# Optimization experiments

Hardware: AMD Instinct MI355X
Metric: run time of the kernel (lower is better)

Reference implementation:

```python
import jax, jax.numpy as jnp
import numpy as np

B, N, H, HEADS = 4, 512, 256, 8
SUBH = H // HEADS
FF = 4 * H
EPS = 1e-5


def _layernorm(x, g, b):
    m = jnp.mean(x, axis=-1, keepdims=True)
    v = jnp.mean(jnp.square(x - m), axis=-1, keepdims=True)
    return (x - m) * jax.lax.rsqrt(v + EPS) * g + b


def setup_inputs() -> dict:
    key = jax.random.key(0)
    ks = jax.random.split(key, 10)
    sc = 0.02
    return {
        "S": jax.random.normal(ks[0], (B, N, H), dtype=jnp.float32),
        "T": jax.random.normal(ks[1], (B, N, N, H), dtype=jnp.float32),
        "masks": jnp.ones((B, N), dtype=bool),
        "Wqk": jax.random.normal(ks[2], (H, HEADS), dtype=jnp.float32) * sc,
        "Wv": jax.random.normal(ks[3], (H, H), dtype=jnp.float32) * sc,
        "bv": jnp.zeros((H,), dtype=jnp.float32),
        "Wo": jax.random.normal(ks[4], (H, H), dtype=jnp.float32) * sc,
        "bo": jnp.zeros((H,), dtype=jnp.float32),
        "g0": jnp.ones((H,), dtype=jnp.float32),
        "beta0": jnp.zeros((H,), dtype=jnp.float32),
        "W1": jax.random.normal(ks[5], (H, FF), dtype=jnp.float32) * sc,
        "b1": jnp.zeros((FF,), dtype=jnp.float32),
        "W2": jax.random.normal(ks[6], (FF, H), dtype=jnp.float32) * sc,
        "b2": jnp.zeros((H,), dtype=jnp.float32),
        "g1": jnp.ones((H,), dtype=jnp.float32),
        "beta1": jnp.zeros((H,), dtype=jnp.float32),
    }


def reference(S, T, masks, Wqk, Wv, bv, Wo, bo, g0, beta0, W1, b1, W2, b2, g1, beta1):
    # pairwise mask: [B,N,N], additive -1000 where masked
    mask2 = masks[:, None, :] & masks[:, :, None]
    add = -1000.0 * (1.0 - mask2.astype(jnp.float32))

    # attention scores: linear projection of pairwise tensor T -> [B, heads, N, N]
    attn = jnp.einsum('bije,eh->bhij', T, Wqk) + add[:, None, :, :]
    attn = jax.nn.softmax(attn, axis=-1)

    # values: [B, heads, N, subH]
    v = (S @ Wv + bv).reshape(B, N, HEADS, SUBH).transpose(0, 2, 1, 3)
    ctx = jnp.einsum('bhij,bhjd->bhid', attn, v)  # [B, heads, N, subH]
    ctx = ctx.transpose(0, 2, 1, 3).reshape(B, N, H)

    x = jax.nn.relu(ctx @ Wo + bo)
    x = _layernorm(S + x, g0, beta0)

    y = jax.nn.relu(x @ W1 + b1) @ W2 + b2
    out = _layernorm(x + y, g1, beta1)
    return (out, attn)
```

## Files before the change

### kernel.cpp

```cpp
#include <hip/hip_runtime.h>
#include <hip/hip_bf16.h>
#include <cstddef>

#define NB 4
#define NN 512
#define NH 256
#define NHEADS 8
#define NSUBH 32
#define NFF 1024
#define LNEPS 1e-5f

using short8 = __attribute__((ext_vector_type(8))) short;
using f32x4  = __attribute__((ext_vector_type(4))) float;
using fvec4  = __attribute__((ext_vector_type(4))) float;

__device__ __forceinline__ unsigned short f2bf(float x) {
    __hip_bfloat16 h = __float2bfloat16(x);
    return *reinterpret_cast<unsigned short*>(&h);
}

__global__ __launch_bounds__(64) void prep_wqk_kernel(
    const float* __restrict__ Wqk, short8* __restrict__ wqk_bf)
{
    const int lane = threadIdx.x;
    const int n = lane & 15;
    #pragma unroll
    for (int ks = 0; ks < 8; ++ks) {
        short8 v;
        #pragma unroll
        for (int q = 0; q < 8; ++q) {
            const int k = ks * 32 + ((lane >> 4) & 3) * 8 + q;
            v[q] = (n < 8) ? (short)f2bf(Wqk[k * NHEADS + n]) : (short)0;
        }
        wqk_bf[ks * 64 + lane] = v;
    }
}

__global__ __launch_bounds__(256) void vproj_kernel(
    const float* __restrict__ S, const float* __restrict__ Wv,
    const float* __restrict__ bv, float* __restrict__ v_ws)
{
    __shared__ float srow[8][NH];
    const int t = threadIdx.x;
    const int row0 = blockIdx.x * 8;
    #pragma unroll
    for (int r = 0; r < 8; ++r) srow[r][t] = S[(size_t)(row0 + r) * NH + t];
    __syncthreads();

    float acc[8];
    #pragma unroll
    for (int r = 0; r < 8; ++r) acc[r] = 0.0f;
    for (int e = 0; e < NH; e += 4) {
        const float w0 = Wv[(size_t)(e + 0) * NH + t];
        const float w1 = Wv[(size_t)(e + 1) * NH + t];
        const float w2 = Wv[(size_t)(e + 2) * NH + t];
        const float w3 = Wv[(size_t)(e + 3) * NH + t];
        #pragma unroll
        for (int r = 0; r < 8; ++r) {
            const float4 x4 = *(const float4*)&srow[r][e];
            acc[r] = fmaf(x4.x, w0, fmaf(x4.y, w1, fmaf(x4.z, w2, fmaf(x4.w, w3, acc[r]))));
        }
    }
    const float bvc = bv[t];
    const int h = t >> 5, d = t & 31;
    const int b = row0 / NN;
    const int jbase = row0 & (NN - 1);
    #pragma unroll
    for (int r = 0; r < 8; ++r)
        v_ws[((size_t)(b * NHEADS + h) * NN + (size_t)(jbase + r)) * NSUBH + d] = acc[r] + bvc;
}

__global__ __launch_bounds__(256, 4) void scores_kernel(
    const float* __restrict__ T, const short8* __restrict__ wqk_bf,
    float* __restrict__ scores)
{
    __shared__ unsigned short tlds[64 * 256];
    const int t = threadIdx.x;
    const int lane = t & 63, wv = t >> 6;
    const int bi = blockIdx.x >> 3;
    const int jt = blockIdx.x & 7;
    const int jbase = jt * 64;

    const fvec4* Tv = (const fvec4*)(T + ((size_t)bi * NN + jbase) * NH);

    fvec4 ga[16];
    #pragma unroll
    for (int i = 0; i < 16; ++i)
        ga[i] = __builtin_nontemporal_load(&Tv[(size_t)(16 * wv + i) * 64 + lane]);

    short8 bfrag[8];
    #pragma unroll
    for (int ks = 0; ks < 8; ++ks) bfrag[ks] = wqk_bf[ks * 64 + lane];

    #pragma unroll
    for (int i = 0; i < 16; ++i) {
        const int row = 16 * wv + i;
        unsigned short v[4];
        v[0] = f2bf(ga[i][0]); v[1] = f2bf(ga[i][1]);
        v[2] = f2bf(ga[i][2]); v[3] = f2bf(ga[i][3]);
        const int byte = (row * 512 + lane * 8) ^ ((row & 7) << 4);
        *(uint2*)((char*)tlds + byte) = *(const uint2*)v;
    }

    f32x4 acc = {0.0f, 0.0f, 0.0f, 0.0f};
    const int jr = 16 * wv + (lane & 15);
    #pragma unroll
    for (int ks = 0; ks < 8; ++ks) {
        const int byte = (jr * 512 + ks * 64 + (lane >> 4) * 16) ^ ((jr & 7) << 4);
        const short8 af = *(const short8*)((const char*)tlds + byte);
        acc = __builtin_amdgcn_mfma_f32_16x16x32_bf16(af, bfrag[ks], acc, 0, 0, 0);
    }

    const int h = lane & 15;
    if (h < 8) {
        const int b = bi >> 9, i = bi & (NN - 1);
        const int j0 = jbase + 16 * wv + (lane >> 4) * 4;
        float4 st;
        st.x = acc[0]; st.y = acc[1]; st.z = acc[2]; st.w = acc[3];
        *(float4*)&scores[((size_t)(b * NHEADS + h) * NN + i) * NN + j0] = st;
    }
}

__global__ __launch_bounds__(256) void softmax_ctx_kernel(
    const int* __restrict__ masks, const float* __restrict__ v_ws,
    float* __restrict__ attn, float* __restrict__ ctx_out)
{
    __shared__ float sc[NN][9];
    __shared__ float maddv[NN];
    const int t = threadIdx.x;
    const int b = blockIdx.x >> 9;
    const int i = blockIdx.x & (NN - 1);

    const int mi = masks[b * NN + i];
    for (int j = t; j < NN; j += 256)
        maddv[j] = (mi != 0 && masks[b * NN + j] != 0) ? 0.0f : -1000.0f;
    __syncthreads();

    const int h = t >> 5;
    const int l32 = t & 31;
    float* srow = attn + ((size_t)(b * NHEADS + h) * NN + i) * NN;

    float vals[16];
    float m = -1e30f;
    #pragma unroll
    for (int k = 0; k < 4; ++k) {
        const int j0 = 4 * l32 + 128 * k;
        float4 s4 = *(const float4*)&srow[j0];
        const float4 m4 = *(const float4*)&maddv[j0];
        s4.x += m4.x; s4.y += m4.y; s4.z += m4.z; s4.w += m4.w;
        vals[4 * k + 0] = s4.x; vals[4 * k + 1] = s4.y;
        vals[4 * k + 2] = s4.z; vals[4 * k + 3] = s4.w;
        m = fmaxf(m, fmaxf(fmaxf(s4.x, s4.y), fmaxf(s4.z, s4.w)));
    }
    #pragma unroll
    for (int off = 16; off >= 1; off >>= 1) m = fmaxf(m, __shfl_xor(m, off, 32));
    float sum = 0.0f;
    #pragma unroll
    for (int k = 0; k < 16; ++k) {
        const float e = __expf(vals[k] - m);
        vals[k] = e;
        sum += e;
    }
    #pragma unroll
    for (int off = 16; off >= 1; off >>= 1) sum += __shfl_xor(sum, off, 32);
    const float inv = 1.0f / sum;
    #pragma unroll
    for (int k = 0; k < 4; ++k) {
        const int j0 = 4 * l32 + 128 * k;
        float4 p4;
        p4.x = vals[4 * k + 0] * inv; p4.y = vals[4 * k + 1] * inv;
        p4.z = vals[4 * k + 2] * inv; p4.w = vals[4 * k + 3] * inv;
        *(float4*)&srow[j0] = p4;
        sc[j0 + 0][h] = p4.x; sc[j0 + 1][h] = p4.y;
        sc[j0 + 2][h] = p4.z; sc[j0 + 3][h] = p4.w;
    }
    __syncthreads();

    const int d = l32;
    const float* vp = v_ws + (size_t)(b * NHEADS + h) * NN * NSUBH + d;
    float acc = 0.0f;
    #pragma unroll 8
    for (int j = 0; j < NN; ++j)
        acc = fmaf(sc[j][h], vp[(size_t)j * NSUBH], acc);
    ctx_out[(size_t)(b * NN + i) * NH + h * NSUBH + d] = acc;
}

__global__ __launch_bounds__(256) void tail_kernel(
    const float* __restrict__ ctx, const float* __restrict__ S,
    const float* __restrict__ Wo, const float* __restrict__ bo,
    const float* __restrict__ g0, const float* __restrict__ beta0,
    const float* __restrict__ W1, const float* __restrict__ b1,
    const float* __restrict__ W2, const float* __restrict__ b2,
    const float* __restrict__ g1, const float* __restrict__ beta1,
    float* __restrict__ out)
{
    __shared__ float xin[8][NH];
    __shared__ float x1[8][NH];
    __shared__ float ybuf[8][NFF];
    const int t = threadIdx.x;
    const int row0 = blockIdx.x * 8;

    #pragma unroll
    for (int r = 0; r < 8; ++r) xin[r][t] = ctx[(size_t)(row0 + r) * NH + t];
    __syncthreads();

    float acc[8];
    #pragma unroll
    for (int r = 0; r < 8; ++r) acc[r] = 0.0f;
    for (int e = 0; e < NH; e += 4) {
        const float w0 = Wo[(size_t)(e + 0) * NH + t];
        const float w1 = Wo[(size_t)(e + 1) * NH + t];
        const float w2 = Wo[(size_t)(e + 2) * NH + t];
        const float w3 = Wo[(size_t)(e + 3) * NH + t];
        #pragma unroll
        for (int r = 0; r < 8; ++r) {
            const float4 x4 = *(const float4*)&xin[r][e];
            acc[r] = fmaf(x4.x, w0, fmaf(x4.y, w1, fmaf(x4.z, w2, fmaf(x4.w, w3, acc[r]))));
        }
    }
    const float boc = bo[t];
    #pragma unroll
    for (int r = 0; r < 8; ++r) {
        const float xv = fmaxf(acc[r] + boc, 0.0f);
        x1[r][t] = S[(size_t)(row0 + r) * NH + t] + xv;
    }
    __syncthreads();

    {
        const int wv = t >> 6, ln = t & 63;
        #pragma unroll
        for (int rr = 0; rr < 2; ++rr) {
            const int r = wv * 2 + rr;
            float s1 = 0.0f, s2 = 0.0f;
            #pragma unroll
            for (int k = 0; k < 4; ++k) {
                const float z = x1[r][ln + 64 * k];
                s1 += z; s2 += z * z;
            }
            #pragma unroll
            for (int off = 32; off >= 1; off >>= 1) {
                s1 += __shfl_xor(s1, off);
                s2 += __shfl_xor(s2, off);
            }
            const float mu = s1 * (1.0f / NH);
            const float rsig = rsqrtf(s2 * (1.0f / NH) - mu * mu + LNEPS);
            #pragma unroll
            for (int k = 0; k < 4; ++k) {
                const int c = ln + 64 * k;
                x1[r][c] = (x1[r][c] - mu) * rsig * g0[c] + beta0[c];
            }
        }
    }
    __syncthreads();

    float acc2[8][4];
    #pragma unroll
    for (int r = 0; r < 8; ++r)
        #pragma unroll
        for (int q = 0; q < 4; ++q) acc2[r][q] = 0.0f;
    for (int e = 0; e < NH; e += 4) {
        float4 x4[8];
        #pragma unroll
        for (int r = 0; r < 8; ++r) x4[r] = *(const float4*)&x1[r][e];
        #pragma unroll
        for (int q = 0; q < 4; ++q) {
            const float* wc = W1 + (size_t)e * NFF + (t + 256 * q);
            const float w0 = wc[0 * NFF], w1 = wc[1 * NFF], w2 = wc[2 * NFF], w3 = wc[3 * NFF];
            #pragma unroll
            for (int r = 0; r < 8; ++r)
                acc2[r][q] = fmaf(x4[r].x, w0, fmaf(x4[r].y, w1, fmaf(x4[r].z, w2, fmaf(x4[r].w, w3, acc2[r][q]))));
        }
    }
    #pragma unroll
    for (int q = 0; q < 4; ++q) {
        const float b1c = b1[t + 256 * q];
        #pragma unroll
        for (int r = 0; r < 8; ++r)
            ybuf[r][t + 256 * q] = fmaxf(acc2[r][q] + b1c, 0.0f);
    }
    __syncthreads();

    float acc3[8];
    #pragma unroll
    for (int r = 0; r < 8; ++r) acc3[r] = 0.0f;
    for (int f = 0; f < NFF; f += 4) {
        const float w0 = W2[(size_t)(f + 0) * NH + t];
        const float w1 = W2[(size_t)(f + 1) * NH + t];
        const float w2 = W2[(size_t)(f + 2) * NH + t];
        const float w3 = W2[(size_t)(f + 3) * NH + t];
        #pragma unroll
        for (int r = 0; r < 8; ++r) {
            const float4 y4 = *(const float4*)&ybuf[r][f];
            acc3[r] = fmaf(y4.x, w0, fmaf(y4.y, w1, fmaf(y4.z, w2, fmaf(y4.w, w3, acc3[r]))));
        }
    }
    const float b2c = b2[t];
    #pragma unroll
    for (int r = 0; r < 8; ++r)
        xin[r][t] = x1[r][t] + acc3[r] + b2c;
    __syncthreads();

    {
        const int wv = t >> 6, ln = t & 63;
        #pragma unroll
        for (int rr = 0; rr < 2; ++rr) {
            const int r = wv * 2 + rr;
            float s1 = 0.0f, s2 = 0.0f;
            #pragma unroll
            for (int k = 0; k < 4; ++k) {
                const float z = xin[r][ln + 64 * k];
                s1 += z; s2 += z * z;
            }
            #pragma unroll
            for (int off = 32; off >= 1; off >>= 1) {
                s1 += __shfl_xor(s1, off);
                s2 += __shfl_xor(s2, off);
            }
            const float mu = s1 * (1.0f / NH);
            const float rsig = rsqrtf(s2 * (1.0f / NH) - mu * mu + LNEPS);
            #pragma unroll
            for (int k = 0; k < 4; ++k) {
                const int c = ln + 64 * k;
                out[(size_t)(row0 + r) * NH + c] = (xin[r][c] - mu) * rsig * g1[c] + beta1[c];
            }
        }
    }
}

extern "C" void kernel_launch(void* const* d_in, const int* in_sizes, int n_in,
                              void* d_out, int out_size, void* d_ws, size_t ws_size,
                              hipStream_t stream) {
    const float* S     = (const float*)d_in[0];
    const float* T     = (const float*)d_in[1];
    const int*   masks = (const int*)  d_in[2];
    const float* Wqk   = (const float*)d_in[3];
    const float* Wv    = (const float*)d_in[4];
    const float* bv    = (const float*)d_in[5];
    const float* Wo    = (const float*)d_in[6];
    const float* bo    = (const float*)d_in[7];
    const float* g0    = (const float*)d_in[8];
    const float* beta0 = (const float*)d_in[9];
    const float* W1    = (const float*)d_in[10];
    const float* b1    = (const float*)d_in[11];
    const float* W2    = (const float*)d_in[12];
    const float* b2    = (const float*)d_in[13];
    const float* g1    = (const float*)d_in[14];
    const float* beta1 = (const float*)d_in[15];

    float* out      = (float*)d_out;
    float* attn_out = out + (size_t)NB * NN * NH;
    float* v_ws     = (float*)d_ws;
    short8* wqk_bf  = (short8*)((char*)d_ws + (size_t)NB * NHEADS * NN * NSUBH * 4);
    float* ctx      = out;

    prep_wqk_kernel<<<1, 64, 0, stream>>>(Wqk, wqk_bf);
    vproj_kernel<<<NB * NN / 8, 256, 0, stream>>>(S, Wv, bv, v_ws);
    scores_kernel<<<NB * NN * 8, 256, 0, stream>>>(T, wqk_bf, attn_out);
    softmax_ctx_kernel<<<NB * NN, 256, 0, stream>>>(masks, v_ws, attn_out, ctx);
    tail_kernel<<<NB * NN / 8, 256, 0, stream>>>(ctx, S, Wo, bo, g0, beta0,
                                                 W1, b1, W2, b2, g1, beta1, out);
}
```

Measured before the change: 339.7 us.

## Merge Wqk prep into vproj, split ctx reduction over j, use nontemporal stores

Folds the single-block Wqk bf16 preparation into an extra block of the vproj launch, removing one kernel launch. Rewrites the attention-times-V step so each thread covers one head, four output dims and a quarter of the j range. It loads V as float4 and reduces the four partial sums through shared memory. Attention probabilities and the final outputs are now written with nontemporal stores to reduce cache pollution. The trade-offs are an extra barrier and more shared memory in the softmax kernel.

```diff
diff --git a/kernel.cpp b/kernel.cpp
--- a/kernel.cpp
+++ b/kernel.cpp
@@ -19,29 +19,31 @@
     return *reinterpret_cast<unsigned short*>(&h);
 }
 
-__global__ __launch_bounds__(64) void prep_wqk_kernel(
+__global__ __launch_bounds__(256) void vproj_kernel(
+    const float* __restrict__ S, const float* __restrict__ Wv,
+    const float* __restrict__ bv, float* __restrict__ v_ws,
     const float* __restrict__ Wqk, short8* __restrict__ wqk_bf)
 {
-    const int lane = threadIdx.x;
-    const int n = lane & 15;
-    #pragma unroll
-    for (int ks = 0; ks < 8; ++ks) {
-        short8 v;
-        #pragma unroll
-        for (int q = 0; q < 8; ++q) {
-            const int k = ks * 32 + ((lane >> 4) & 3) * 8 + q;
-            v[q] = (n < 8) ? (short)f2bf(Wqk[k * NHEADS + n]) : (short)0;
-        }
-        wqk_bf[ks * 64 + lane] = v;
-    }
-}
-
-__global__ __launch_bounds__(256) void vproj_kernel(
-    const float* __restrict__ S, const float* __restrict__ Wv,
-    const float* __restrict__ bv, float* __restrict__ v_ws)
-{
+    const int t = threadIdx.x;
+    if (blockIdx.x == NB * NN / 8) {
+        if (t < 64) {
+            const int lane = t;
+            const int n = lane & 15;
+            #pragma unroll
+            for (int ks = 0; ks < 8; ++ks) {
+                short8 v;
+                #pragma unroll
+                for (int q = 0; q < 8; ++q) {
+                    const int k = ks * 32 + ((lane >> 4) & 3) * 8 + q;
+                    v[q] = (n < 8) ? (short)f2bf(Wqk[k * NHEADS + n]) : (short)0;
+                }
+                wqk_bf[ks * 64 + lane] = v;
+            }
+        }
+        return;
+    }
+
     __shared__ float srow[8][NH];
-    const int t = threadIdx.x;
     const int row0 = blockIdx.x * 8;
     #pragma unroll
     for (int r = 0; r < 8; ++r) srow[r][t] = S[(size_t)(row0 + r) * NH + t];
@@ -127,6 +129,7 @@
 {
     __shared__ float sc[NN][9];
     __shared__ float maddv[NN];
+    __shared__ float cpart[4][NHEADS][NSUBH];
     const int t = threadIdx.x;
     const int b = blockIdx.x >> 9;
     const int i = blockIdx.x & (NN - 1);
@@ -167,22 +170,33 @@
     #pragma unroll
     for (int k = 0; k < 4; ++k) {
         const int j0 = 4 * l32 + 128 * k;
-        float4 p4;
-        p4.x = vals[4 * k + 0] * inv; p4.y = vals[4 * k + 1] * inv;
-        p4.z = vals[4 * k + 2] * inv; p4.w = vals[4 * k + 3] * inv;
-        *(float4*)&srow[j0] = p4;
-        sc[j0 + 0][h] = p4.x; sc[j0 + 1][h] = p4.y;
-        sc[j0 + 2][h] = p4.z; sc[j0 + 3][h] = p4.w;
-    }
+        fvec4 p4;
+        p4[0] = vals[4 * k + 0] * inv; p4[1] = vals[4 * k + 1] * inv;
+        p4[2] = vals[4 * k + 2] * inv; p4[3] = vals[4 * k + 3] * inv;
+        __builtin_nontemporal_store(p4, (fvec4*)&srow[j0]);
+        sc[j0 + 0][h] = p4[0]; sc[j0 + 1][h] = p4[1];
+        sc[j0 + 2][h] = p4[2]; sc[j0 + 3][h] = p4[3];
+    }
+    __syncthreads();
+
+    const int h2 = t & 7, dg = (t >> 3) & 7, jq = t >> 6;
+    const float* vbase = v_ws + (size_t)(b * NHEADS + h2) * NN * NSUBH + dg * 4;
+    float4 pacc = make_float4(0.0f, 0.0f, 0.0f, 0.0f);
+    #pragma unroll 8
+    for (int j = jq * 128; j < jq * 128 + 128; ++j) {
+        const float p = sc[j][h2];
+        const float4 v4 = *(const float4*)(vbase + (size_t)j * NSUBH);
+        pacc.x = fmaf(p, v4.x, pacc.x);
+        pacc.y = fmaf(p, v4.y, pacc.y);
+        pacc.z = fmaf(p, v4.z, pacc.z);
+        pacc.w = fmaf(p, v4.w, pacc.w);
+    }
+    *(float4*)&cpart[jq][h2][dg * 4] = pacc;
     __syncthreads();
 
     const int d = l32;
-    const float* vp = v_ws + (size_t)(b * NHEADS + h) * NN * NSUBH + d;
-    float acc = 0.0f;
-    #pragma unroll 8
-    for (int j = 0; j < NN; ++j)
-        acc = fmaf(sc[j][h], vp[(size_t)j * NSUBH], acc);
-    ctx_out[(size_t)(b * NN + i) * NH + h * NSUBH + d] = acc;
+    const float s = cpart[0][h][d] + cpart[1][h][d] + cpart[2][h][d] + cpart[3][h][d];
+    ctx_out[(size_t)(b * NN + i) * NH + h * NSUBH + d] = s;
 }
 
 __global__ __launch_bounds__(256) void tail_kernel(
@@ -321,7 +335,8 @@
             #pragma unroll
             for (int k = 0; k < 4; ++k) {
                 const int c = ln + 64 * k;
-                out[(size_t)(row0 + r) * NH + c] = (xin[r][c] - mu) * rsig * g1[c] + beta1[c];
+                const float o = (xin[r][c] - mu) * rsig * g1[c] + beta1[c];
+                __builtin_nontemporal_store(o, &out[(size_t)(row0 + r) * NH + c]);
             }
         }
     }
@@ -353,8 +368,7 @@
     short8* wqk_bf  = (short8*)((char*)d_ws + (size_t)NB * NHEADS * NN * NSUBH * 4);
     float* ctx      = out;
 
-    prep_wqk_kernel<<<1, 64, 0, stream>>>(Wqk, wqk_bf);
-    vproj_kernel<<<NB * NN / 8, 256, 0, stream>>>(S, Wv, bv, v_ws);
+    vproj_kernel<<<NB * NN / 8 + 1, 256, 0, stream>>>(S, Wv, bv, v_ws, Wqk, wqk_bf);
     scores_kernel<<<NB * NN * 8, 256, 0, stream>>>(T, wqk_bf, attn_out);
     softmax_ctx_kernel<<<NB * NN, 256, 0, stream>>>(masks, v_ws, attn_out, ctx);
     tail_kernel<<<NB * NN / 8, 256, 0, stream>>>(ctx, S, Wo, bo, g0, beta0,
```

After: 402.7 us. 1.19x slower.
